# Optimization experiments

Hardware: AMD Instinct MI355X
Metric: run time of the kernel (lower is better)

## Reference

```python
import jax, jax.numpy as jnp
import numpy as np

B, NS, NC, D = 32, 1024, 1024, 256   # batch, sentence len, comment len, latent/embedding dim
K = 128                              # co-attention latent size (self.k)
CLIP_R = 2.0
EPS = 1e-5

def _norm(x):
    return jnp.sqrt(jnp.maximum(jnp.sum(x * x, -1, keepdims=True), 1e-15))

def artanh(x):
    x = jnp.clip(x, -1 + 1e-5, 1 - 1e-5)
    return 0.5 * (jnp.log1p(x) - jnp.log1p(-x))

# ---------- Poincare ball, c = 1 ----------
def p_logmap0(y):
    yn = _norm(y)
    return artanh(yn) * y / yn

def p_expmap0(u):
    un = _norm(u)
    return jnp.tanh(un) * u / un

def mobius_add(x, y):
    xy = jnp.sum(x * y, -1, keepdims=True)
    x2 = jnp.sum(x * x, -1, keepdims=True)
    y2 = jnp.sum(y * y, -1, keepdims=True)
    num = (1 + 2 * xy + y2) * x + (1 - x2) * y
    den = jnp.maximum(1 + 2 * xy + x2 * y2, 1e-15)
    return num / den

def mobius_matvec(m, x):
    # geoopt convention: result = 'x @ m^T' transported through the ball
    xn = _norm(x)
    mx = jnp.matmul(x, jnp.swapaxes(m, -1, -2))
    mxn = _norm(mx)
    return jnp.tanh(mxn / xn * artanh(xn)) * mx / mxn

# ---------- Lorentz hyperboloid, k = 1 ----------
def l_expmap0_space(v_space):
    # exp map at origin of a tangent vector with zero time component
    vn = _norm(v_space)
    return jnp.concatenate([jnp.cosh(vn), jnp.sinh(vn) * v_space / vn], -1)

def euclid_to_lorentz(x):
    xn = _norm(x) + EPS
    x = x * jnp.minimum(1.0, CLIP_R / xn)  # clip_r feature clipping
    return l_expmap0_space(x)              # F.pad time=0 then expmap0

def lorentz_linear(x, W, b):
    y = jnp.matmul(x, W.T) + b
    space = y[..., 1:]
    time = jnp.sqrt(jnp.sum(space * space, -1, keepdims=True) + 1.0)
    return jnp.concatenate([time, space], -1)

def lorentz_act(x):
    space = jax.nn.gelu(x[..., 1:], approximate=False)
    time = jnp.sqrt(jnp.sum(space * space, -1, keepdims=True) + 1.0)
    return jnp.concatenate([time, space], -1)

def lorentz_to_poincare(x):
    return x[..., 1:] / (x[..., :1] + 1.0)

def l_inner(u, v):
    return -u[..., :1] * v[..., :1] + jnp.sum(u[..., 1:] * v[..., 1:], -1, keepdims=True)

def centroid(x, w):
    avg = jnp.matmul(w, x)  # weighted Lorentz average, then renormalize to hyperboloid
    den = jnp.sqrt(jnp.maximum(jnp.abs(l_inner(avg, avg)), 1e-8))
    return avg / den

def l_logmap0_space(x):
    t = jnp.maximum(x[..., :1], 1 + 1e-7)
    return jnp.arccosh(t) * x[..., 1:] / _norm(x[..., 1:])

def lorentz_concat(x, y):
    z = jnp.concatenate([l_logmap0_space(x), l_logmap0_space(y)], -1)
    return l_expmap0_space(z)


def setup_inputs() -> dict:
    key = jax.random.key(0)
    ks = jax.random.split(key, 8)
    sentence = jax.random.normal(ks[0], (B, NS, D), jnp.float32)
    comment = jax.random.normal(ks[1], (B, NC, D), jnp.float32)
    comment = 0.9 * comment / (_norm(comment) + 1.0)  # valid Poincare-ball points
    w = lambda k, o, i: jax.random.normal(k, (o, i), jnp.float32) * 0.05
    return {
        'sentence_rep': sentence,
        'comment_rep': comment,
        'Wl_W': w(ks[2], D + 1, D + 1), 'Wl_b': jnp.zeros((D + 1,), jnp.float32),
        'Wc_W': w(ks[3], K + 1, D + 1), 'Wc_b': jnp.zeros((K + 1,), jnp.float32),
        'Ws_W': w(ks[4], K + 1, D + 1), 'Ws_b': jnp.zeros((K + 1,), jnp.float32),
        'whs': jax.random.uniform(ks[5], (1, K), jnp.float32),
        'whc': jax.random.uniform(ks[6], (1, K), jnp.float32),
    }


def reference(sentence_rep, comment_rep, Wl_W, Wl_b, Wc_W, Wc_b, Ws_W, Ws_b, whs, whc):
    T = lambda a: jnp.swapaxes(a, -1, -2)
    # Fourier mixing (real part, as torch .float() on complex)
    s = jnp.fft.fft2(sentence_rep).real.astype(jnp.float32)
    c = jnp.fft.fft2(p_logmap0(comment_rep)).real.astype(jnp.float32)
    Ls = euclid_to_lorentz(s)            # [B,NS,D+1]
    Lc = euclid_to_lorentz(c)            # [B,NC,D+1]
    L = lorentz_linear(Lc, Wl_W, Wl_b)   # [B,NC,D+1]
    L = lorentz_act(jnp.einsum('bnd,bmd->bnm', Ls, L))  # [B,NS,NC] affinity
    # Ws(sentence) and Wc(comment) in Poincare coords (computed once; original recomputes)
    Hs_a = lorentz_to_poincare(lorentz_linear(Ls, Ws_W, Ws_b))  # [B,NS,K]
    Hc_a = lorentz_to_poincare(lorentz_linear(Lc, Wc_W, Wc_b))  # [B,NC,K]
    Hs_b = mobius_matvec(T(Hc_a), L)          # [B,NS,K]
    Hs = mobius_add(Hs_a, Hs_b)
    Hs = p_expmap0(jax.nn.gelu(p_logmap0(Hs), approximate=False))
    Hc_b = mobius_matvec(T(Hs_a), T(L))       # [B,NC,K]
    Hc = mobius_add(T(Hc_a), T(Hc_b))         # [B,K,NC]
    Hc = p_expmap0(jax.nn.gelu(p_logmap0(Hc), approximate=False))
    As = jax.nn.softmax(T(mobius_matvec(whs, Hs)), axis=-1)     # [B,1,NS]
    Ac = jax.nn.softmax(T(mobius_matvec(whc, T(Hc))), axis=-1)  # [B,1,NC]
    co_s = centroid(Ls, As)                   # [B,1,D+1]
    co_c = centroid(Lc, Ac)                   # [B,1,D+1]
    co_sc = jnp.squeeze(lorentz_concat(co_s, co_c), axis=1)     # [B,2D+1]
    return co_sc, As, Ac
```

## Files before the change

kernel.cpp:

```cpp
#include <hip/hip_runtime.h>
#include <cstdint>
#include <math.h>

#define NBATCH 32
#define NSQ 1024
#define NCQ 1024
#define DDIM 256
#define DP 257
#define KQ 128
#define KPAD 288
#define NFOLD 640
#define KF2 640
#define MXSPLIT 4194304

typedef __attribute__((ext_vector_type(8))) short short8;
typedef __attribute__((ext_vector_type(4))) float floatx4;

__device__ __forceinline__ float bf2f(ushort u) { return __uint_as_float(((uint)u) << 16); }
__device__ __forceinline__ ushort f2bf(float f) {
    uint u = __float_as_uint(f);
    return (ushort)((u + 0x7FFFu + ((u >> 16) & 1u)) >> 16);
}
__device__ __forceinline__ void gload16(const void* g, void* l) {
    __builtin_amdgcn_global_load_lds(
        (const __attribute__((address_space(1))) void*)g,
        (__attribute__((address_space(3))) void*)l,
        16, 0, 0);
}
__device__ __forceinline__ float artanh_clip(float x) {
    x = fminf(fmaxf(x, -1.0f + 1e-5f), 1.0f - 1e-5f);
    return 0.5f * (log1pf(x) - log1pf(-x));
}
__device__ __forceinline__ float gelu_f(float x) {
    return 0.5f * x * (1.0f + erff(x * 0.70710678118654752440f));
}
__device__ __forceinline__ float waveRedSum(float v) {
#pragma unroll
    for (int o = 32; o > 0; o >>= 1) v += __shfl_down(v, o, 64);
    return __shfl(v, 0, 64);
}
__device__ __forceinline__ float blockRedSum(float v, float* buf) {
    int lane = threadIdx.x & 63, wid = threadIdx.x >> 6;
#pragma unroll
    for (int o = 32; o > 0; o >>= 1) v += __shfl_down(v, o, 64);
    __syncthreads();
    if (lane == 0) buf[wid] = v;
    __syncthreads();
    int nw = blockDim.x >> 6;
    float s = buf[0];
    for (int i = 1; i < nw; i++) s += buf[i];
    return s;
}
__device__ __forceinline__ float blockRedMax(float v, float* buf) {
    int lane = threadIdx.x & 63, wid = threadIdx.x >> 6;
#pragma unroll
    for (int o = 32; o > 0; o >>= 1) v = fmaxf(v, __shfl_down(v, o, 64));
    __syncthreads();
    if (lane == 0) buf[wid] = v;
    __syncthreads();
    int nw = blockDim.x >> 6;
    float s = buf[0];
    for (int i = 1; i < nw; i++) s = fmaxf(s, buf[i]);
    return s;
}

template <bool A_NN, bool B_NN, bool OUT_BF16, bool BIAS, bool ATOMIC, int NSPLIT, bool DUAL>
__global__ __launch_bounds__(256) void mfma_gemm(
    const short* __restrict__ A, int lda, int64_t sA,
    const short* __restrict__ B, int ldb, int64_t sB,
    void* __restrict__ Cv, int ldc, int64_t sC,
    const float* __restrict__ bias, int M, int N, int K,
    const short* __restrict__ A1, const short* __restrict__ B1, int64_t cOff1,
    const float* __restrict__ biasB)
{
    __shared__ short As[128][32];
    __shared__ short Bs[128][32];
    const int zz = blockIdx.z;
    int zb, ks, half;
    if (DUAL) { half = zz & 1; zb = zz >> 1; ks = 0; }
    else      { zb = zz / NSPLIT; ks = zz - zb * NSPLIT; half = 0; }
    const short* Ap = (DUAL && half) ? A1 : A;
    const short* Bp = (DUAL && half) ? B1 : B;
    Ap += (int64_t)zb * sA;
    Bp += (int64_t)zb * sB;
    const int kper = K / NSPLIT;
    const int kbeg = ks * kper, kend = kbeg + kper;
    const int m0 = blockIdx.y * 128, n0 = blockIdx.x * 128;
    const int t = threadIdx.x;
    const int lane = t & 63, w = t >> 6;
    const int wm = (w & 1) * 64, wn = (w >> 1) * 64;
    floatx4 acc[4][4] = {};
    for (int k0 = kbeg; k0 < kend; k0 += 32) {
        if (!A_NN) {
            int r = t >> 2, c8 = (t & 3) * 8;
            const short* ap = Ap + (int64_t)(m0 + r) * lda + k0 + c8;
            gload16(ap, &As[r][c8]);
            gload16(ap + (int64_t)64 * lda, &As[r + 64][c8]);
        } else {
            int r2 = t >> 4, c8 = (t & 15) * 8;
            int kk = 2 * r2;
            const ushort* a0 = (const ushort*)Ap + (int64_t)(k0 + kk) * lda + m0 + c8;
            uint4 v0 = *(const uint4*)a0;
            uint4 v1 = *(const uint4*)(a0 + lda);
            const ushort* p0 = (const ushort*)&v0;
            const ushort* p1 = (const ushort*)&v1;
#pragma unroll
            for (int i = 0; i < 8; i++) {
                uint pk = (uint)p0[i] | ((uint)p1[i] << 16);
                *(uint*)&As[c8 + i][kk] = pk;
            }
        }
        if (!B_NN) {
            int r = t >> 2, c8 = (t & 3) * 8;
            const short* bp = Bp + (int64_t)(n0 + r) * ldb + k0 + c8;
            gload16(bp, &Bs[r][c8]);
            gload16(bp + (int64_t)64 * ldb, &Bs[r + 64][c8]);
        } else {
            int r2 = t >> 4, c8 = (t & 15) * 8;
            int kk = 2 * r2;
            const ushort* b0 = (const ushort*)Bp + (int64_t)(k0 + kk) * ldb + n0 + c8;
            uint4 v0 = *(const uint4*)b0;
            uint4 v1 = *(const uint4*)(b0 + ldb);
            const ushort* p0 = (const ushort*)&v0;
            const ushort* p1 = (const ushort*)&v1;
#pragma unroll
            for (int i = 0; i < 8; i++) {
                uint pk = (uint)p0[i] | ((uint)p1[i] << 16);
                *(uint*)&Bs[c8 + i][kk] = pk;
            }
        }
        __syncthreads();
        short8 af[4], bfv[4];
#pragma unroll
        for (int i = 0; i < 4; i++)
            af[i] = *(const short8*)&As[wm + 16 * i + (lane & 15)][8 * (lane >> 4)];
#pragma unroll
        for (int i = 0; i < 4; i++)
            bfv[i] = *(const short8*)&Bs[wn + 16 * i + (lane & 15)][8 * (lane >> 4)];
#pragma unroll
        for (int i = 0; i < 4; i++)
#pragma unroll
            for (int j = 0; j < 4; j++)
                acc[i][j] = __builtin_amdgcn_mfma_f32_16x16x32_bf16(af[i], bfv[j], acc[i][j], 0, 0, 0);
        __syncthreads();
    }
    const int q = lane >> 4, c = lane & 15;
    int64_t cbase = (int64_t)zb * sC + ((DUAL && half) ? cOff1 : 0);
    if (NSPLIT > 1 && !ATOMIC) cbase += (int64_t)ks * cOff1;
    const float* bsel = (BIAS && biasB && zb) ? biasB : bias;
#pragma unroll
    for (int j = 0; j < 4; j++) {
        int col = n0 + wn + 16 * j + c;
        float bv = BIAS ? bsel[col] : 0.0f;
#pragma unroll
        for (int i = 0; i < 4; i++) {
            int rowb = m0 + wm + 16 * i + 4 * q;
#pragma unroll
            for (int r = 0; r < 4; r++) {
                float v = acc[i][j][r] + bv;
                int64_t idx = cbase + (int64_t)(rowb + r) * ldc + col;
                if (ATOMIC)       atomicAdd((float*)Cv + idx, v);
                else if (OUT_BF16) ((ushort*)Cv)[idx] = f2bf(v);
                else               ((float*)Cv)[idx] = v;
            }
        }
    }
}

__global__ __launch_bounds__(256) void genconst_kernel(
    ushort* CS1c, ushort* CS1s, ushort* C2, ushort* S2,
    const float* __restrict__ WlW, const float* __restrict__ WsW, const float* __restrict__ WcW,
    ushort* Wl, ushort* Ws, ushort* Wc)
{
    int blk = blockIdx.x, t = threadIdx.x;
    if (blk < 3200) {
        int idx = blk * 256 + t;
        int hs = idx >= 409600;
        int e = idx - hs * 409600;
        int n = e / KF2, k = e - n * KF2;
        float v = 0.0f;
        if (k <= 512) {
            int p = (n * k) & 1023;
            float ang = (6.28318530717958647692f / 1024.0f) * (float)p;
            v = hs ? ((k == 0) ? 0.0f : -sinf(ang)) : cosf(ang);
        }
        (hs ? CS1s : CS1c)[e] = f2bf(v);
    } else if (blk < 3456) {
        int idx = (blk - 3200) * 256 + t;
        int d = idx >> 8, j = idx & 255;
        int p = (d * j) & 255;
        float ang = (6.28318530717958647692f / 256.0f) * (float)p;
        C2[idx] = f2bf(cosf(ang));
        S2[idx] = f2bf(sinf(ang));
    } else {
        int r = blk - 3456;
        const float* src; ushort* dst; int srow;
        if (r < 256)      { src = WlW; dst = Wl + r * KPAD;        srow = r + 1; }
        else if (r < 384) { src = WsW; dst = Ws + (r - 256) * KPAD; srow = r - 256 + 1; }
        else              { src = WcW; dst = Wc + (r - 384) * KPAD; srow = r - 384 + 1; }
        dst[t] = (t < DP) ? f2bf(src[(int64_t)srow * DP + t]) : (ushort)0;
        if (t < KPAD - 256) {
            int t2 = t + 256;
            dst[t2] = (t2 < DP) ? f2bf(src[(int64_t)srow * DP + t2]) : (ushort)0;
        }
    }
}

__global__ __launch_bounds__(256) void prep_fold_kernel(const float* __restrict__ sent,
                                                        const float* __restrict__ comm,
                                                        ushort* __restrict__ XC, ushort* __restrict__ XS) {
    int bp = blockIdx.x;
    int z = blockIdx.y * 4 + (threadIdx.x >> 6);
    int lane = threadIdx.x & 63;
    int m2 = (1024 - bp) & 1023;
    const float* base = (z < 32) ? sent + (int64_t)z * 262144 : comm + (int64_t)(z - 32) * 262144;
    float4 a = *(const float4*)(base + bp * 256 + 4 * lane);
    float4 b = *(const float4*)(base + m2 * 256 + 4 * lane);
    if (z >= 32) {
        float s1 = waveRedSum(a.x * a.x + a.y * a.y + a.z * a.z + a.w * a.w);
        float yn1 = sqrtf(fmaxf(s1, 1e-15f));
        float f1 = artanh_clip(yn1) / yn1;
        a.x *= f1; a.y *= f1; a.z *= f1; a.w *= f1;
        float s2 = waveRedSum(b.x * b.x + b.y * b.y + b.z * b.z + b.w * b.w);
        float yn2 = sqrtf(fmaxf(s2, 1e-15f));
        float f2v = artanh_clip(yn2) / yn2;
        b.x *= f2v; b.y *= f2v; b.z *= f2v; b.w *= f2v;
    }
    int64_t o = ((int64_t)z * NFOLD + bp) * 256 + 4 * lane;
    bool single = (bp == 0) || (bp == 512);
    ushort4 oc;
    oc.x = f2bf(single ? a.x : a.x + b.x);
    oc.y = f2bf(single ? a.y : a.y + b.y);
    oc.z = f2bf(single ? a.z : a.z + b.z);
    oc.w = f2bf(single ? a.w : a.w + b.w);
    *(ushort4*)(XC + o) = oc;
    if (!single) {
        ushort4 os;
        os.x = f2bf(a.x - b.x); os.y = f2bf(a.y - b.y);
        os.z = f2bf(a.z - b.z); os.w = f2bf(a.w - b.w);
        *(ushort4*)(XS + o) = os;
    }
}

__global__ __launch_bounds__(256) void e2l_kernel(const ushort* __restrict__ YcYs,
                                                  ushort* __restrict__ Lsb, ushort* __restrict__ Lcb) {
    int64_t row = (int64_t)blockIdx.x * 4 + (threadIdx.x >> 6);
    int lane = threadIdx.x & 63;
    int z = (int)(row >> 10), n = (int)(row & 1023);
    int np = (n <= 512) ? n : 1024 - n;
    float sgn = (n <= 512) ? 1.0f : -1.0f;
    const ushort* base = YcYs + (int64_t)z * 327680 + np * 256 + 4 * lane;
    ushort4 uc = *(const ushort4*)base;
    ushort4 us = *(const ushort4*)(base + 163840);
    float v0 = bf2f(uc.x) + sgn * bf2f(us.x);
    float v1 = bf2f(uc.y) + sgn * bf2f(us.y);
    float v2 = bf2f(uc.z) + sgn * bf2f(us.z);
    float v3 = bf2f(uc.w) + sgn * bf2f(us.w);
    float s = waveRedSum(v0 * v0 + v1 * v1 + v2 * v2 + v3 * v3);
    float xn = sqrtf(fmaxf(s, 1e-15f)) + 1e-5f;
    float sc = fminf(1.0f, 2.0f / xn);
    float s2 = fmaxf(s * sc * sc, 1e-15f);
    float vn = sqrtf(s2);
    float e = expf(vn);
    float ei = 1.0f / e;
    float shv = (vn < 1e-4f) ? 1.0f : (e - ei) * 0.5f / vn;
    float fac = shv * sc;
    ushort* ob = (row < 32768 ? Lsb + row * KPAD : Lcb + (row - 32768) * KPAD);
    ob[1 + 4 * lane + 0] = f2bf(fac * v0);
    ob[1 + 4 * lane + 1] = f2bf(fac * v1);
    ob[1 + 4 * lane + 2] = f2bf(fac * v2);
    ob[1 + 4 * lane + 3] = f2bf(fac * v3);
    if (lane == 0) ob[0] = f2bf((e + ei) * 0.5f);
    if (lane < KPAD - DP) ob[DP + lane] = 0;
}

__global__ __launch_bounds__(256) void lnorm_kernel(ushort* __restrict__ Llin_bf) {
    int64_t row = (int64_t)blockIdx.x * 4 + (threadIdx.x >> 6);
    int lane = threadIdx.x & 63;
    ushort* ob = Llin_bf + row * KPAD;
    float s = 0.f;
#pragma unroll
    for (int i = 0; i < 4; i++) { float v = bf2f(ob[1 + 4 * lane + i]); s += v * v; }
    s = waveRedSum(s);
    if (lane == 0) ob[0] = f2bf(sqrtf(s + 1.0f));
    if (lane < KPAD - DP) ob[DP + lane] = 0;
}

__global__ __launch_bounds__(256) void poinc2_kernel(ushort* __restrict__ Hcat) {
    int64_t row = (int64_t)blockIdx.x * 4 + (threadIdx.x >> 6);
    int lane = threadIdx.x & 63;
    ushort* r = Hcat + row * KQ;
    ushort2 u = *(ushort2*)&r[2 * lane];
    float v0 = bf2f(u.x), v1 = bf2f(u.y);
    float s = waveRedSum(v0 * v0 + v1 * v1);
    float inv = 1.0f / (sqrtf(s + 1.0f) + 1.0f);
    ushort2 o; o.x = f2bf(v0 * inv); o.y = f2bf(v1 * inv);
    *(ushort2*)&r[2 * lane] = o;
}

__global__ __launch_bounds__(256) void lact_kernel(ushort* __restrict__ Lmat, float* __restrict__ xnrow) {
    __shared__ float red[4];
    int64_t row = blockIdx.x; int t = threadIdx.x;
    ushort* r = Lmat + row * (int64_t)NCQ;
    ushort4 u = *(ushort4*)&r[4 * t];
    float v[4] = {bf2f(u.x), bf2f(u.y), bf2f(u.z), bf2f(u.w)};
    float g[4]; float s = 0.f;
#pragma unroll
    for (int i = 0; i < 4; i++) {
        int idx = 4 * t + i;
        if (idx > 0) { g[i] = gelu_f(v[i]); s += g[i] * g[i]; } else g[i] = 0.f;
    }
    s = blockRedSum(s, red);
    if (t == 0) g[0] = sqrtf(1.0f + s);
    ushort4 o; o.x = f2bf(g[0]); o.y = f2bf(g[1]); o.z = f2bf(g[2]); o.w = f2bf(g[3]);
    *(ushort4*)&r[4 * t] = o;
    if (t == 0) xnrow[row] = sqrtf(fmaxf(1.0f + 2.0f * s, 1e-15f));
}

__global__ void tmat_kernel(const ushort* __restrict__ in, ushort* __restrict__ outp) {
    __shared__ ushort tile[32][33];
    int z = blockIdx.z;
    int r0 = blockIdx.x * 32, c0 = blockIdx.y * 32;
    const ushort* ib = in + (int64_t)z * 1048576;
    ushort* ob = outp + (int64_t)z * 1048576;
    int tx = threadIdx.x, ty = threadIdx.y;
    for (int i = 0; i < 32; i += 8) tile[ty + i][tx] = ib[(r0 + ty + i) * 1024 + c0 + tx];
    __syncthreads();
    for (int i = 0; i < 32; i += 8) ob[(c0 + ty + i) * 1024 + r0 + tx] = tile[tx][ty + i];
}

__global__ __launch_bounds__(256) void colnormA_kernel(const ushort* __restrict__ Lmat, float* __restrict__ part) {
    int b = blockIdx.x, chunk = blockIdx.y, t = threadIdx.x;
    const ushort* base = Lmat + (int64_t)b * NSQ * NCQ + (int64_t)chunk * 128 * NCQ + 4 * t;
    float s0 = 0.f, s1 = 0.f, s2 = 0.f, s3 = 0.f;
    for (int n = 0; n < 128; n++) {
        ushort4 u = *(const ushort4*)(base + (int64_t)n * NCQ);
        float a = bf2f(u.x), bb = bf2f(u.y), c = bf2f(u.z), d = bf2f(u.w);
        s0 += a * a; s1 += bb * bb; s2 += c * c; s3 += d * d;
    }
    float4 o = {s0, s1, s2, s3};
    *(float4*)(part + ((int64_t)(b * 8 + chunk)) * 4096 + 4 * t) = o;
}
__global__ __launch_bounds__(256) void cnscale_kernel(const float* __restrict__ part,
                                                      float* __restrict__ mxcT) {
    int b = blockIdx.x; int m = blockIdx.y * 256 + threadIdx.x;
    const float* p = part + (int64_t)b * 8 * 4096 + m;
    float s = 0.f;
#pragma unroll
    for (int c = 0; c < 8; c++) s += p[c * 4096];
    float xn = sqrtf(fmaxf(s, 1e-15f));
    float* base = mxcT + (int64_t)b * KQ * NCQ + m;
    const float* base2 = base + MXSPLIT;
    float sm = 0.f;
    for (int j = 0; j < KQ; j++) {
        float v = base[j * NCQ] + base2[j * NCQ];
        base[j * NCQ] = v;
        sm += v * v;
    }
    float mxn = sqrtf(fmaxf(sm, 1e-15f));
    float fac = tanhf(mxn / xn * artanh_clip(xn)) / mxn;
    for (int j = 0; j < KQ; j++) base[j * NCQ] *= fac;
}

__global__ __launch_bounds__(64) void rowops_s_kernel(
    const ushort* __restrict__ Hsa, const float* __restrict__ mxs,
    const float* __restrict__ xnrow, const float* __restrict__ whs,
    float* __restrict__ logits)
{
    int64_t row = blockIdx.x; int t = threadIdx.x;
    const ushort* p = Hsa + row * KQ;
    const float* q = mxs + row * KQ;
    float p0 = bf2f(p[t]), p1 = bf2f(p[t + 64]);
    float q0 = q[t] + q[t + MXSPLIT], q1 = q[t + 64] + q[t + 64 + MXSPLIT];
    float mxn = sqrtf(fmaxf(waveRedSum(q0 * q0 + q1 * q1), 1e-15f));
    float xn = xnrow[row];
    float fac = tanhf(mxn / xn * artanh_clip(xn)) / mxn;
    float y0 = fac * q0, y1 = fac * q1;
    float xy = waveRedSum(p0 * y0 + p1 * y1);
    float x2 = waveRedSum(p0 * p0 + p1 * p1);
    float y2 = waveRedSum(y0 * y0 + y1 * y1);
    float ca = 1.f + 2.f * xy + y2, cb = 1.f - x2;
    float den = fmaxf(1.f + 2.f * xy + x2 * y2, 1e-15f);
    float h0 = (ca * p0 + cb * y0) / den, h1 = (ca * p1 + cb * y1) / den;
    float hn = sqrtf(fmaxf(waveRedSum(h0 * h0 + h1 * h1), 1e-15f));
    float uf = artanh_clip(hn) / hn;
    float g0 = gelu_f(uf * h0), g1 = gelu_f(uf * h1);
    float gn = sqrtf(fmaxf(waveRedSum(g0 * g0 + g1 * g1), 1e-15f));
    float ef = tanhf(gn) / gn;
    float H0 = ef * g0, H1 = ef * g1;
    float dot = waveRedSum(H0 * whs[t] + H1 * whs[t + 64]);
    float Hn = sqrtf(fmaxf(waveRedSum(H0 * H0 + H1 * H1), 1e-15f));
    float mxn2 = sqrtf(fmaxf(dot * dot, 1e-15f));
    float lg = tanhf(mxn2 / Hn * artanh_clip(Hn)) * dot / mxn2;
    if (t == 0) logits[row] = lg;
}

__global__ void thsa_kernel(const ushort* __restrict__ in, ushort* __restrict__ outp) {
    __shared__ ushort tile[32][33];
    int z = blockIdx.z;
    int n0 = blockIdx.x * 32, j0 = blockIdx.y * 32;
    const ushort* ib = in + (int64_t)z * 131072;
    ushort* ob = outp + (int64_t)z * 131072;
    int tx = threadIdx.x, ty = threadIdx.y;
    for (int i = 0; i < 32; i += 8) tile[ty + i][tx] = ib[(n0 + ty + i) * 128 + j0 + tx];
    __syncthreads();
    for (int i = 0; i < 32; i += 8) ob[(j0 + ty + i) * 1024 + n0 + tx] = tile[tx][ty + i];
}

__global__ __launch_bounds__(256) void rowops_c_kernel(const ushort* __restrict__ HcAT, float* __restrict__ y) {
    __shared__ float red[4];
    int64_t row = blockIdx.x;
    const ushort* xbase = HcAT + row * (int64_t)NCQ;
    float* yr = y + row * (int64_t)NCQ;
    int t = threadIdx.x;
    float xv[4], yv[4];
    float xy = 0.f, x2 = 0.f, y2 = 0.f;
#pragma unroll
    for (int i = 0; i < 4; i++) {
        int m = t + 256 * i;
        xv[i] = bf2f(xbase[m]); yv[i] = yr[m];
        xy += xv[i] * yv[i]; x2 += xv[i] * xv[i]; y2 += yv[i] * yv[i];
    }
    xy = blockRedSum(xy, red);
    x2 = blockRedSum(x2, red);
    y2 = blockRedSum(y2, red);
    float ca = 1.f + 2.f * xy + y2, cb = 1.f - x2;
    float den = fmaxf(1.f + 2.f * xy + x2 * y2, 1e-15f);
    float h[4]; float hn2 = 0.f;
#pragma unroll
    for (int i = 0; i < 4; i++) { h[i] = (ca * xv[i] + cb * yv[i]) / den; hn2 += h[i] * h[i]; }
    hn2 = blockRedSum(hn2, red);
    float hn = sqrtf(fmaxf(hn2, 1e-15f));
    float uf = artanh_clip(hn) / hn;
    float g[4]; float gn2 = 0.f;
#pragma unroll
    for (int i = 0; i < 4; i++) { g[i] = gelu_f(uf * h[i]); gn2 += g[i] * g[i]; }
    gn2 = blockRedSum(gn2, red);
    float gn = sqrtf(fmaxf(gn2, 1e-15f));
    float ef = tanhf(gn) / gn;
#pragma unroll
    for (int i = 0; i < 4; i++) yr[t + 256 * i] = ef * g[i];
}

__global__ __launch_bounds__(256) void logitsc_kernel(const float* __restrict__ Hc, const float* __restrict__ whc, float* __restrict__ lgc) {
    int b = blockIdx.x; int m = blockIdx.y * 256 + threadIdx.x;
    const float* base = Hc + (int64_t)b * KQ * NCQ + m;
    float s1 = 0.f, s2 = 0.f;
    for (int j = 0; j < KQ; j++) { float v = base[j * NCQ]; s1 += v * whc[j]; s2 += v * v; }
    float xn = sqrtf(fmaxf(s2, 1e-15f));
    float mxn = sqrtf(fmaxf(s1 * s1, 1e-15f));
    lgc[b * NCQ + m] = tanhf(mxn / xn * artanh_clip(xn)) * s1 / mxn;
}

__global__ __launch_bounds__(256) void softmax_kernel(const float* __restrict__ lg, float* __restrict__ outp) {
    __shared__ float red[4];
    int b = blockIdx.x; int t = threadIdx.x;
    const float* x = lg + b * 1024;
    float v[4]; float m = -1e30f;
#pragma unroll
    for (int i = 0; i < 4; i++) { v[i] = x[t + 256 * i]; m = fmaxf(m, v[i]); }
    m = blockRedMax(m, red);
    float s = 0.f;
#pragma unroll
    for (int i = 0; i < 4; i++) { v[i] = expf(v[i] - m); s += v[i]; }
    s = blockRedSum(s, red);
    float inv = 1.0f / s;
#pragma unroll
    for (int i = 0; i < 4; i++) outp[b * 1024 + t + 256 * i] = v[i] * inv;
}

__global__ __launch_bounds__(320) void centroidA_kernel(
    const ushort* __restrict__ Lsb, const ushort* __restrict__ Lcb,
    const float* __restrict__ As, const float* __restrict__ Ac,
    float* __restrict__ part)
{
    int b = blockIdx.x;
    int which = blockIdx.y;
    int chunk = blockIdx.z;
    const ushort* L = which ? Lcb : Lsb;
    const float* w = which ? Ac : As;
    int t = threadIdx.x;
    if (t >= DP) return;
    const ushort* Lb = L + (int64_t)b * NSQ * KPAD + (int64_t)chunk * 128 * KPAD + t;
    const float* wb = w + b * NSQ + chunk * 128;
    float s = 0.f;
    for (int n = 0; n < 128; n++) s += wb[n] * bf2f(Lb[(int64_t)n * KPAD]);
    part[((int64_t)((b * 2 + which) * 8 + chunk)) * 264 + t] = s;
}
__global__ __launch_bounds__(320) void centroidB_kernel(
    const float* __restrict__ part, float* __restrict__ co_s, float* __restrict__ co_c)
{
    int b = blockIdx.x;
    int which = blockIdx.y;
    int t = threadIdx.x;
    if (t >= DP) return;
    const float* p = part + (int64_t)(b * 2 + which) * 8 * 264 + t;
    float s = 0.f;
#pragma unroll
    for (int c = 0; c < 8; c++) s += p[c * 264];
    (which ? co_c : co_s)[b * DP + t] = s;
}

__global__ __launch_bounds__(256) void final_kernel(const float* __restrict__ co_s, const float* __restrict__ co_c, float* __restrict__ outp) {
    __shared__ float red[4];
    int b = blockIdx.x, t = threadIdx.x;
    float zmine[2];
    for (int w = 0; w < 2; w++) {
        const float* co = (w ? co_c : co_s) + b * DP;
        float at = co[0];
        float asp = co[1 + t];
        float ssp = blockRedSum(asp * asp, red);
        float li = ssp - at * at;
        float den = sqrtf(fmaxf(fabsf(li), 1e-8f));
        float xt = at / den, xsp = asp / den;
        float s2 = blockRedSum(xsp * xsp, red);
        float nrm = sqrtf(fmaxf(s2, 1e-15f));
        float ac = acoshf(fmaxf(xt, 1.0f + 1e-7f));
        zmine[w] = ac * xsp / nrm;
    }
    float vn2 = blockRedSum(zmine[0] * zmine[0] + zmine[1] * zmine[1], red);
    float vn = sqrtf(fmaxf(vn2, 1e-15f));
    float sc = sinhf(vn) / vn;
    if (t == 0) outp[b * 513] = coshf(vn);
    outp[b * 513 + 1 + t] = sc * zmine[0];
    outp[b * 513 + 1 + 256 + t] = sc * zmine[1];
}

extern "C" void kernel_launch(void* const* d_in, const int* in_sizes, int n_in,
                              void* d_out, int out_size, void* d_ws, size_t ws_size,
                              hipStream_t stream)
{
    const float* sent = (const float*)d_in[0];
    const float* comm = (const float*)d_in[1];
    const float* WlW  = (const float*)d_in[2];
    const float* Wlb  = (const float*)d_in[3];
    const float* WcW  = (const float*)d_in[4];
    const float* Wcb  = (const float*)d_in[5];
    const float* WsW  = (const float*)d_in[6];
    const float* Wsb  = (const float*)d_in[7];
    const float* whs  = (const float*)d_in[8];
    const float* whc  = (const float*)d_in[9];
    float* out = (float*)d_out;
    (void)in_sizes; (void)n_in; (void)out_size; (void)ws_size;

    float* ws = (float*)d_ws;
    size_t off = 0;
    auto take = [&](size_t n) { float* p = ws + off; off += n; return p; };
    float*  xnrow = take(32768);
    float*  lgs   = take(32768);
    float*  lgc   = take(32768);
    float*  co_s  = take(8224);
    float*  co_c  = take(8224);
    ushort* Ls_bf = (ushort*)take(4718592);
    ushort* Lc_bf = (ushort*)take(4718592);
    ushort* Wl_bf = (ushort*)take(36864);
    ushort* Ws_bf = (ushort*)take(18432);
    ushort* Wc_bf = (ushort*)take(18432);
    ushort* HsA_bf = (ushort*)take(2097152);
    ushort* HcA_bf = (ushort*)take(2097152);
    float*  part_cn   = take(1048576);
    float*  part_cent = take(135168);
    ushort* LmatT_bf  = (ushort*)take(16777216);
    float*  F     = take(33554432);

    ushort* XC_bf   = (ushort*)F;
    ushort* XS_bf   = (ushort*)(F + 5242880);
    ushort* Ff_bf   = (ushort*)(F + 10485760);
    ushort* CS1c    = (ushort*)(F + 20971520);
    ushort* CS1s    = (ushort*)(F + 21176320);
    ushort* C2_bf   = (ushort*)(F + 21381120);
    ushort* S2_bf   = (ushort*)(F + 21413888);
    ushort* YcYs    = (ushort*)F;
    ushort* Lmat_bf = (ushort*)F;
    ushort* Llin_bf = (ushort*)(F + 29360128);
    float*  mx      = F + 16777216;
    ushort* HsAT    = (ushort*)(F + 25165824);
    ushort* HcAT    = (ushort*)(F + 27262976);

    float* AsOut = out + 16416;
    float* AcOut = out + 16416 + 32768;

    dim3 blk(256);
    const short* NUL = nullptr;

    genconst_kernel<<<3968, 256, 0, stream>>>(CS1c, CS1s, C2_bf, S2_bf, WlW, WsW, WcW, Wl_bf, Ws_bf, Wc_bf);

    prep_fold_kernel<<<dim3(513, 16), blk, 0, stream>>>(sent, comm, XC_bf, XS_bf);
    mfma_gemm<false,false,true,false,false,1,true><<<dim3(5,2,128), blk, 0, stream>>>(
        (const short*)C2_bf,256,0, (const short*)XC_bf,256,(int64_t)NFOLD*256, Ff_bf,1280,(int64_t)256*1280,
        nullptr, 256,NFOLD,256, (const short*)S2_bf, (const short*)XS_bf, 640, nullptr);
    mfma_gemm<false,false,true,false,false,1,true><<<dim3(2,5,128), blk, 0, stream>>>(
        (const short*)CS1c,KF2,0, (const short*)Ff_bf,1280,(int64_t)256*1280, YcYs,256,327680,
        nullptr, NFOLD,256,KF2, (const short*)CS1s, (const short*)(Ff_bf+640), 163840, nullptr);
    e2l_kernel<<<16384, blk, 0, stream>>>(YcYs, Ls_bf, Lc_bf);

    mfma_gemm<false,false,true,true,false,1,false><<<dim3(2,256,1), blk, 0, stream>>>(
        (const short*)Lc_bf,KPAD,0, (const short*)Wl_bf,KPAD,0, (void*)(Llin_bf+1),KPAD,0,
        Wlb+1, 32768,256,KPAD, NUL, NUL, 0, nullptr);
    lnorm_kernel<<<8192, blk, 0, stream>>>(Llin_bf);

    mfma_gemm<false,false,true,false,false,1,false><<<dim3(8,8,32), blk, 0, stream>>>(
        (const short*)Ls_bf,KPAD,294912, (const short*)Llin_bf,KPAD,294912, Lmat_bf,1024,1048576,
        nullptr, 1024,1024,KPAD, NUL, NUL, 0, nullptr);
    lact_kernel<<<32768, blk, 0, stream>>>(Lmat_bf, xnrow);
    tmat_kernel<<<dim3(32,32,32), dim3(32,8), 0, stream>>>(Lmat_bf, LmatT_bf);
    colnormA_kernel<<<dim3(32,8), blk, 0, stream>>>(Lmat_bf, part_cn);

    mfma_gemm<false,false,true,true,false,1,false><<<dim3(1,256,2), blk, 0, stream>>>(
        (const short*)Ls_bf,KPAD,9437184, (const short*)Ws_bf,KPAD,36864, HsA_bf,128,4194304,
        Wsb+1, 32768,128,KPAD, NUL, NUL, 0, Wcb+1);
    poinc2_kernel<<<16384, blk, 0, stream>>>(HsA_bf);

    thsa_kernel<<<dim3(32,4,64), dim3(32,8), 0, stream>>>(HsA_bf, HsAT);

    mfma_gemm<false,false,false,false,false,2,false><<<dim3(1,8,64), blk, 0, stream>>>(
        (const short*)Lmat_bf,1024,1048576, (const short*)HcAT,1024,131072, mx,128,131072,
        nullptr, 1024,128,1024, NUL, NUL, MXSPLIT, nullptr);
    rowops_s_kernel<<<32768, 64, 0, stream>>>(HsA_bf, mx, xnrow, whs, lgs);

    mfma_gemm<false,false,false,false,false,2,false><<<dim3(8,1,64), blk, 0, stream>>>(
        (const short*)HsAT,1024,131072, (const short*)LmatT_bf,1024,1048576, mx,1024,131072,
        nullptr, 128,1024,1024, NUL, NUL, MXSPLIT, nullptr);
    cnscale_kernel<<<dim3(32,4), blk, 0, stream>>>(part_cn, mx);
    rowops_c_kernel<<<4096, blk, 0, stream>>>(HcAT, mx);
    logitsc_kernel<<<dim3(32,4), blk, 0, stream>>>(mx, whc, lgc);

    softmax_kernel<<<64, blk, 0, stream>>>(lgs, AsOut);
    centroidA_kernel<<<dim3(32,2,8), 320, 0, stream>>>(Ls_bf, Lc_bf, AsOut, AcOut, part_cent);
    centroidB_kernel<<<dim3(32,2), 320, 0, stream>>>(part_cent, co_s, co_c);
    final_kernel<<<32, blk, 0, stream>>>(co_s, co_c, out);
}
```

Measured before the change: 565.8 us.

## Fuse column scaling into rowops_c and collapse reductions algebraically in row kernels

The column-scaling kernel now computes only a per-column factor instead of writing back the summed and scaled mx matrix twice. rowops_c applies that factor while it reads the split partial sums, so two full passes over the 16 MB mx buffer go away. Both row kernels now use one wave per row with batched wave reductions, and the norms of h, H and y are derived algebraically from xy, x2 and y2 instead of being reduced again. This cuts shuffle and sync work, but the algebraic norms can differ slightly in rounding from direct summation.

```diff
diff --git a/kernel.cpp b/kernel.cpp
--- a/kernel.cpp
+++ b/kernel.cpp
@@ -38,6 +38,23 @@
 #pragma unroll
     for (int o = 32; o > 0; o >>= 1) v += __shfl_down(v, o, 64);
     return __shfl(v, 0, 64);
+}
+__device__ __forceinline__ void waveRedSum3(float& a, float& b, float& c) {
+#pragma unroll
+    for (int o = 32; o > 0; o >>= 1) {
+        a += __shfl_down(a, o, 64);
+        b += __shfl_down(b, o, 64);
+        c += __shfl_down(c, o, 64);
+    }
+    a = __shfl(a, 0, 64); b = __shfl(b, 0, 64); c = __shfl(c, 0, 64);
+}
+__device__ __forceinline__ void waveRedSum2(float& a, float& b) {
+#pragma unroll
+    for (int o = 32; o > 0; o >>= 1) {
+        a += __shfl_down(a, o, 64);
+        b += __shfl_down(b, o, 64);
+    }
+    a = __shfl(a, 0, 64); b = __shfl(b, 0, 64);
 }
 __device__ __forceinline__ float blockRedSum(float v, float* buf) {
     int lane = threadIdx.x & 63, wid = threadIdx.x >> 6;
@@ -217,11 +234,12 @@
     float4 a = *(const float4*)(base + bp * 256 + 4 * lane);
     float4 b = *(const float4*)(base + m2 * 256 + 4 * lane);
     if (z >= 32) {
-        float s1 = waveRedSum(a.x * a.x + a.y * a.y + a.z * a.z + a.w * a.w);
+        float s1 = a.x * a.x + a.y * a.y + a.z * a.z + a.w * a.w;
+        float s2 = b.x * b.x + b.y * b.y + b.z * b.z + b.w * b.w;
+        waveRedSum2(s1, s2);
         float yn1 = sqrtf(fmaxf(s1, 1e-15f));
         float f1 = artanh_clip(yn1) / yn1;
         a.x *= f1; a.y *= f1; a.z *= f1; a.w *= f1;
-        float s2 = waveRedSum(b.x * b.x + b.y * b.y + b.z * b.z + b.w * b.w);
         float yn2 = sqrtf(fmaxf(s2, 1e-15f));
         float f2v = artanh_clip(yn2) / yn2;
         b.x *= f2v; b.y *= f2v; b.z *= f2v; b.w *= f2v;
@@ -341,58 +359,65 @@
     float4 o = {s0, s1, s2, s3};
     *(float4*)(part + ((int64_t)(b * 8 + chunk)) * 4096 + 4 * t) = o;
 }
-__global__ __launch_bounds__(256) void cnscale_kernel(const float* __restrict__ part,
-                                                      float* __restrict__ mxcT) {
+__global__ __launch_bounds__(256) void colfac_kernel(const float* __restrict__ part,
+                                                     const float* __restrict__ mxcT,
+                                                     float* __restrict__ fac_c) {
     int b = blockIdx.x; int m = blockIdx.y * 256 + threadIdx.x;
     const float* p = part + (int64_t)b * 8 * 4096 + m;
     float s = 0.f;
 #pragma unroll
     for (int c = 0; c < 8; c++) s += p[c * 4096];
     float xn = sqrtf(fmaxf(s, 1e-15f));
-    float* base = mxcT + (int64_t)b * KQ * NCQ + m;
+    const float* base = mxcT + (int64_t)b * KQ * NCQ + m;
     const float* base2 = base + MXSPLIT;
     float sm = 0.f;
     for (int j = 0; j < KQ; j++) {
         float v = base[j * NCQ] + base2[j * NCQ];
-        base[j * NCQ] = v;
         sm += v * v;
     }
     float mxn = sqrtf(fmaxf(sm, 1e-15f));
-    float fac = tanhf(mxn / xn * artanh_clip(xn)) / mxn;
-    for (int j = 0; j < KQ; j++) base[j * NCQ] *= fac;
-}
-
-__global__ __launch_bounds__(64) void rowops_s_kernel(
+    fac_c[b * NCQ + m] = tanhf(mxn / xn * artanh_clip(xn)) / mxn;
+}
+
+__global__ __launch_bounds__(256) void rowops_s_kernel(
     const ushort* __restrict__ Hsa, const float* __restrict__ mxs,
     const float* __restrict__ xnrow, const float* __restrict__ whs,
     float* __restrict__ logits)
 {
-    int64_t row = blockIdx.x; int t = threadIdx.x;
+    int64_t row = (int64_t)blockIdx.x * 4 + (threadIdx.x >> 6);
+    int lane = threadIdx.x & 63;
     const ushort* p = Hsa + row * KQ;
     const float* q = mxs + row * KQ;
-    float p0 = bf2f(p[t]), p1 = bf2f(p[t + 64]);
-    float q0 = q[t] + q[t + MXSPLIT], q1 = q[t + 64] + q[t + 64 + MXSPLIT];
-    float mxn = sqrtf(fmaxf(waveRedSum(q0 * q0 + q1 * q1), 1e-15f));
+    float p0 = bf2f(p[lane]), p1 = bf2f(p[lane + 64]);
+    float q0 = q[lane] + q[lane + MXSPLIT];
+    float q1 = q[lane + 64] + q[lane + 64 + MXSPLIT];
+    float r1 = q0 * q0 + q1 * q1;
+    float r2 = p0 * q0 + p1 * q1;
+    float r3 = p0 * p0 + p1 * p1;
+    waveRedSum3(r1, r2, r3);
+    float mxn = sqrtf(fmaxf(r1, 1e-15f));
     float xn = xnrow[row];
     float fac = tanhf(mxn / xn * artanh_clip(xn)) / mxn;
-    float y0 = fac * q0, y1 = fac * q1;
-    float xy = waveRedSum(p0 * y0 + p1 * y1);
-    float x2 = waveRedSum(p0 * p0 + p1 * p1);
-    float y2 = waveRedSum(y0 * y0 + y1 * y1);
+    float xy = fac * r2;
+    float x2 = r3;
+    float y2 = fac * fac * r1;
     float ca = 1.f + 2.f * xy + y2, cb = 1.f - x2;
     float den = fmaxf(1.f + 2.f * xy + x2 * y2, 1e-15f);
-    float h0 = (ca * p0 + cb * y0) / den, h1 = (ca * p1 + cb * y1) / den;
-    float hn = sqrtf(fmaxf(waveRedSum(h0 * h0 + h1 * h1), 1e-15f));
+    float h0 = (ca * p0 + cb * fac * q0) / den, h1 = (ca * p1 + cb * fac * q1) / den;
+    float hn2 = (ca * ca * x2 + 2.f * ca * cb * xy + cb * cb * y2) / (den * den);
+    float hn = sqrtf(fmaxf(hn2, 1e-15f));
     float uf = artanh_clip(hn) / hn;
     float g0 = gelu_f(uf * h0), g1 = gelu_f(uf * h1);
-    float gn = sqrtf(fmaxf(waveRedSum(g0 * g0 + g1 * g1), 1e-15f));
+    float r4 = g0 * g0 + g1 * g1;
+    float r5 = g0 * whs[lane] + g1 * whs[lane + 64];
+    waveRedSum2(r4, r5);
+    float gn = sqrtf(fmaxf(r4, 1e-15f));
     float ef = tanhf(gn) / gn;
-    float H0 = ef * g0, H1 = ef * g1;
-    float dot = waveRedSum(H0 * whs[t] + H1 * whs[t + 64]);
-    float Hn = sqrtf(fmaxf(waveRedSum(H0 * H0 + H1 * H1), 1e-15f));
+    float dot = ef * r5;
+    float Hn = sqrtf(fmaxf(ef * ef * r4, 1e-15f));
     float mxn2 = sqrtf(fmaxf(dot * dot, 1e-15f));
     float lg = tanhf(mxn2 / Hn * artanh_clip(Hn)) * dot / mxn2;
-    if (t == 0) logits[row] = lg;
+    if (lane == 0) logits[row] = lg;
 }
 
 __global__ void thsa_kernel(const ushort* __restrict__ in, ushort* __restrict__ outp) {
@@ -407,39 +432,58 @@
     for (int i = 0; i < 32; i += 8) ob[(j0 + ty + i) * 1024 + n0 + tx] = tile[tx][ty + i];
 }
 
-__global__ __launch_bounds__(256) void rowops_c_kernel(const ushort* __restrict__ HcAT, float* __restrict__ y) {
-    __shared__ float red[4];
-    int64_t row = blockIdx.x;
-    const ushort* xbase = HcAT + row * (int64_t)NCQ;
-    float* yr = y + row * (int64_t)NCQ;
-    int t = threadIdx.x;
-    float xv[4], yv[4];
+__global__ __launch_bounds__(256) void rowops_c_kernel(const ushort* __restrict__ HcAT,
+                                                       float* __restrict__ mx,
+                                                       const float* __restrict__ fac_c) {
+    int64_t row = (int64_t)blockIdx.x * 4 + (threadIdx.x >> 6);
+    int lane = threadIdx.x & 63;
+    int b = (int)(row >> 7);
+    const ushort* xb = HcAT + row * (int64_t)NCQ + 16 * lane;
+    float* yb = mx + row * (int64_t)NCQ + 16 * lane;
+    const float* fb = fac_c + b * NCQ + 16 * lane;
+    float xv[16], yv[16];
+    {
+        uint4 u0 = *(const uint4*)xb;
+        uint4 u1 = *(const uint4*)(xb + 8);
+        const ushort* pu0 = (const ushort*)&u0;
+        const ushort* pu1 = (const ushort*)&u1;
+#pragma unroll
+        for (int i = 0; i < 8; i++) { xv[i] = bf2f(pu0[i]); xv[8 + i] = bf2f(pu1[i]); }
+    }
+#pragma unroll
+    for (int i = 0; i < 16; i += 4) {
+        float4 v1 = *(const float4*)(yb + i);
+        float4 v2 = *(const float4*)(yb + i + MXSPLIT);
+        float4 fv = *(const float4*)(fb + i);
+        yv[i + 0] = fv.x * (v1.x + v2.x);
+        yv[i + 1] = fv.y * (v1.y + v2.y);
+        yv[i + 2] = fv.z * (v1.z + v2.z);
+        yv[i + 3] = fv.w * (v1.w + v2.w);
+    }
     float xy = 0.f, x2 = 0.f, y2 = 0.f;
 #pragma unroll
-    for (int i = 0; i < 4; i++) {
-        int m = t + 256 * i;
-        xv[i] = bf2f(xbase[m]); yv[i] = yr[m];
-        xy += xv[i] * yv[i]; x2 += xv[i] * xv[i]; y2 += yv[i] * yv[i];
-    }
-    xy = blockRedSum(xy, red);
-    x2 = blockRedSum(x2, red);
-    y2 = blockRedSum(y2, red);
+    for (int i = 0; i < 16; i++) { xy += xv[i] * yv[i]; x2 += xv[i] * xv[i]; y2 += yv[i] * yv[i]; }
+    waveRedSum3(xy, x2, y2);
     float ca = 1.f + 2.f * xy + y2, cb = 1.f - x2;
     float den = fmaxf(1.f + 2.f * xy + x2 * y2, 1e-15f);
-    float h[4]; float hn2 = 0.f;
-#pragma unroll
-    for (int i = 0; i < 4; i++) { h[i] = (ca * xv[i] + cb * yv[i]) / den; hn2 += h[i] * h[i]; }
-    hn2 = blockRedSum(hn2, red);
+    float hn2 = (ca * ca * x2 + 2.f * ca * cb * xy + cb * cb * y2) / (den * den);
     float hn = sqrtf(fmaxf(hn2, 1e-15f));
     float uf = artanh_clip(hn) / hn;
-    float g[4]; float gn2 = 0.f;
-#pragma unroll
-    for (int i = 0; i < 4; i++) { g[i] = gelu_f(uf * h[i]); gn2 += g[i] * g[i]; }
-    gn2 = blockRedSum(gn2, red);
+    float g[16]; float gn2 = 0.f;
+#pragma unroll
+    for (int i = 0; i < 16; i++) {
+        float h = (ca * xv[i] + cb * yv[i]) / den;
+        g[i] = gelu_f(uf * h);
+        gn2 += g[i] * g[i];
+    }
+    gn2 = waveRedSum(gn2);
     float gn = sqrtf(fmaxf(gn2, 1e-15f));
     float ef = tanhf(gn) / gn;
 #pragma unroll
-    for (int i = 0; i < 4; i++) yr[t + 256 * i] = ef * g[i];
+    for (int i = 0; i < 16; i += 4) {
+        float4 o = {ef * g[i], ef * g[i + 1], ef * g[i + 2], ef * g[i + 3]};
+        *(float4*)(yb + i) = o;
+    }
 }
 
 __global__ __launch_bounds__(256) void logitsc_kernel(const float* __restrict__ Hc, const float* __restrict__ whc, float* __restrict__ lgc) {
@@ -547,6 +591,7 @@
     size_t off = 0;
     auto take = [&](size_t n) { float* p = ws + off; off += n; return p; };
     float*  xnrow = take(32768);
+    float*  fac_c = take(32768);
     float*  lgs   = take(32768);
     float*  lgc   = take(32768);
     float*  co_s  = take(8224);
@@ -616,13 +661,13 @@
     mfma_gemm<false,false,false,false,false,2,false><<<dim3(1,8,64), blk, 0, stream>>>(
         (const short*)Lmat_bf,1024,1048576, (const short*)HcAT,1024,131072, mx,128,131072,
         nullptr, 1024,128,1024, NUL, NUL, MXSPLIT, nullptr);
-    rowops_s_kernel<<<32768, 64, 0, stream>>>(HsA_bf, mx, xnrow, whs, lgs);
+    rowops_s_kernel<<<8192, blk, 0, stream>>>(HsA_bf, mx, xnrow, whs, lgs);
 
     mfma_gemm<false,false,false,false,false,2,false><<<dim3(8,1,64), blk, 0, stream>>>(
         (const short*)HsAT,1024,131072, (const short*)LmatT_bf,1024,1048576, mx,1024,131072,
         nullptr, 128,1024,1024, NUL, NUL, MXSPLIT, nullptr);
-    cnscale_kernel<<<dim3(32,4), blk, 0, stream>>>(part_cn, mx);
-    rowops_c_kernel<<<4096, blk, 0, stream>>>(HcAT, mx);
+    colfac_kernel<<<dim3(32,4), blk, 0, stream>>>(part_cn, mx, fac_c);
+    rowops_c_kernel<<<1024, blk, 0, stream>>>(HcAT, mx, fac_c);
     logitsc_kernel<<<dim3(32,4), blk, 0, stream>>>(mx, whc, lgc);
 
     softmax_kernel<<<64, blk, 0, stream>>>(lgs, AsOut);
```

Measured after the change: 550.0 us. 2.8% less time.
